# Kernel tuning notes

Measured on AMD Instinct MI355X. Metric: run time of the kernel, lower is better.

Reference implementation:

```python
import jax, jax.numpy as jnp
import numpy as np

EPS = 1e-5

def _layer_norm(x, w):
    mu = jnp.mean(x, axis=-1, keepdims=True)
    var = jnp.mean(jnp.square(x - mu), axis=-1, keepdims=True)
    return (x - mu) * jax.lax.rsqrt(var + EPS) * w

def setup_inputs() -> dict:
    key = jax.random.key(0)
    ks = jax.random.split(key, 5)
    B, T, C, H = 2, 2048, 1024, 16
    std = 0.02
    return {
        "x": jax.random.normal(ks[0], (B, T, C), dtype=jnp.float32),
        "ln1_w": jnp.ones((C,), dtype=jnp.float32),
        "w_attn": jax.random.normal(ks[1], (C, 3 * C), dtype=jnp.float32) * std,
        "w_proj": jax.random.normal(ks[2], (C, C), dtype=jnp.float32) * std,
        "ln2_w": jnp.ones((C,), dtype=jnp.float32),
        "w_fc": jax.random.normal(ks[3], (C, 4 * C), dtype=jnp.float32) * std,
        "w_cproj": jax.random.normal(ks[4], (4 * C, C), dtype=jnp.float32) * std,
    }

def reference(x, ln1_w, w_attn, w_proj, ln2_w, w_fc, w_cproj):
    B, T, C = x.shape
    H = 16
    Dh = C // H
    # --- causal self-attention on ln1(x) ---
    h = _layer_norm(x, ln1_w)
    qkv = h @ w_attn                      # [B,T,3C]
    q, k, v = jnp.split(qkv, 3, axis=-1)
    # [B,T,C] -> [B,H,T,Dh]
    q = q.reshape(B, T, H, Dh).transpose(0, 2, 1, 3)
    k = k.reshape(B, T, H, Dh).transpose(0, 2, 1, 3)
    v = v.reshape(B, T, H, Dh).transpose(0, 2, 1, 3)
    # NOTE: original scales by full embed dim C**-0.5, not head_dim**-0.5
    scores = jnp.einsum('bhqd,bhkd->bhqk', q, k) * (C ** -0.5)
    causal = jnp.tril(jnp.ones((T, T), dtype=bool))
    scores = jnp.where(causal, scores, -jnp.inf)
    probs = jax.nn.softmax(scores, axis=-1)  # dropout=0.0 (eval)
    y = jnp.einsum('bhqk,bhkd->bhqd', probs, v)
    y = y.transpose(0, 2, 1, 3).reshape(B, T, C)
    x = x + y @ w_proj
    # --- MLP on ln2(x) ---
    h = _layer_norm(x, ln2_w)
    x = x + jax.nn.relu(h @ w_fc) @ w_cproj
    return x
```

## Files before the change

### kernel.cpp

```cpp
#include <hip/hip_runtime.h>

typedef __attribute__((ext_vector_type(8))) __bf16 bf16x8;
typedef __attribute__((ext_vector_type(4))) float f32x4;
typedef __attribute__((ext_vector_type(8))) unsigned short u16x8;
typedef __attribute__((ext_vector_type(4))) unsigned short u16x4;
typedef unsigned short u16;

__device__ __forceinline__ u16 f2bf(float f) {
  return __builtin_bit_cast(u16, (__bf16)f);
}
__device__ __forceinline__ float bf2f(u16 u) {
  return __builtin_bit_cast(float, ((unsigned)u) << 16);
}

__device__ __forceinline__ f32x4 mfma16(bf16x8 a, bf16x8 b, f32x4 c) {
  return __builtin_amdgcn_mfma_f32_16x16x32_bf16(a, b, c, 0, 0, 0);
}

__device__ __forceinline__ void gl_lds16(const void* g, void* l) {
  __builtin_amdgcn_global_load_lds(
      (const __attribute__((address_space(1))) unsigned int*)g,
      (__attribute__((address_space(3))) unsigned int*)l, 16, 0, 0);
}

__device__ __forceinline__ f32x4 fmax4(f32x4 a, f32x4 b) {
  f32x4 r;
  r[0] = fmaxf(a[0], b[0]); r[1] = fmaxf(a[1], b[1]);
  r[2] = fmaxf(a[2], b[2]); r[3] = fmaxf(a[3], b[3]);
  return r;
}

__global__ __launch_bounds__(256) void convT_all(const float* __restrict__ w0,
                                                 u16* __restrict__ o0,
                                                 const float* __restrict__ w1,
                                                 u16* __restrict__ o1,
                                                 const float* __restrict__ w2,
                                                 u16* __restrict__ o2,
                                                 const float* __restrict__ w3,
                                                 u16* __restrict__ o3) {
  __shared__ float tile[64][65];
  const int id = blockIdx.x;
  const float* in;
  u16* outT;
  int K, N, bx, by;
  if (id < 768) { in = w0; outT = o0; K = 1024; N = 3072; bx = id & 15; by = id >> 4; }
  else if (id < 1024) { const int j = id - 768; in = w1; outT = o1; K = 1024; N = 1024; bx = j & 15; by = j >> 4; }
  else if (id < 2048) { const int j = id - 1024; in = w2; outT = o2; K = 1024; N = 4096; bx = j & 15; by = j >> 4; }
  else { const int j = id - 2048; in = w3; outT = o3; K = 4096; N = 1024; bx = j & 63; by = j >> 6; }
  const int t = threadIdx.x;
  const int tk = bx * 64, tn = by * 64;
  const int lk = t >> 4, ln = (t & 15) * 4;
#pragma unroll
  for (int r = 0; r < 4; ++r) {
    const int k = lk + r * 16;
    const float4 v = *(const float4*)(in + (size_t)(tk + k) * N + tn + ln);
    tile[k][ln + 0] = v.x; tile[k][ln + 1] = v.y;
    tile[k][ln + 2] = v.z; tile[k][ln + 3] = v.w;
  }
  __syncthreads();
  const int sn = t >> 2, sk = (t & 3) * 4;
#pragma unroll
  for (int j = 0; j < 4; ++j) {
    const int k = sk + j * 16;
    ushort4 o;
    o.x = f2bf(tile[k + 0][sn]); o.y = f2bf(tile[k + 1][sn]);
    o.z = f2bf(tile[k + 2][sn]); o.w = f2bf(tile[k + 3][sn]);
    *(ushort4*)(outT + (size_t)(tn + sn) * K + tk + k) = o;
  }
}

__global__ __launch_bounds__(256) void vtrans(const u16* __restrict__ qkvb,
                                              u16* __restrict__ vT) {
  __shared__ u16 tile[64][72];
  const int t = threadIdx.x;
  const int tt0 = blockIdx.x * 64;
  const int bh = blockIdx.y;
  const int b = bh >> 4, h = bh & 15;
  const u16* src = qkvb + (size_t)(b * 2048 + tt0) * 3072 + 2048 + h * 64;
  {
    const int tl = t >> 2, d0 = (t & 3) * 16;
    const u16x8 a0 = *(const u16x8*)(src + (size_t)tl * 3072 + d0);
    const u16x8 a1 = *(const u16x8*)(src + (size_t)tl * 3072 + d0 + 8);
    *(u16x8*)(&tile[tl][d0]) = a0;
    *(u16x8*)(&tile[tl][d0 + 8]) = a1;
  }
  __syncthreads();
  {
    const int dh = t >> 2, t0 = (t & 3) * 16;
    u16x8 o0, o1;
#pragma unroll
    for (int jj = 0; jj < 8; ++jj) {
      o0[jj] = tile[t0 + jj][dh];
      o1[jj] = tile[t0 + 8 + jj][dh];
    }
    u16* dst = vT + ((size_t)bh * 64 + dh) * 2048 + tt0 + t0;
    *(u16x8*)dst = o0;
    *(u16x8*)(dst + 8) = o1;
  }
}

__global__ __launch_bounds__(256) void ln_bf16(const float* __restrict__ x,
                                               const float* __restrict__ wgt,
                                               u16* __restrict__ out) {
  const int row = blockIdx.x, t = threadIdx.x;
  const float4 v = ((const float4*)(x + (size_t)row * 1024))[t];
  float s = v.x + v.y + v.z + v.w;
  float q = v.x * v.x + v.y * v.y + v.z * v.z + v.w * v.w;
#pragma unroll
  for (int d = 32; d; d >>= 1) { s += __shfl_xor(s, d); q += __shfl_xor(q, d); }
  __shared__ float sb[8];
  const int wv = t >> 6;
  if ((t & 63) == 0) { sb[wv] = s; sb[4 + wv] = q; }
  __syncthreads();
  s = sb[0] + sb[1] + sb[2] + sb[3];
  q = sb[4] + sb[5] + sb[6] + sb[7];
  const float mu = s * (1.f / 1024.f);
  const float rstd = rsqrtf(q * (1.f / 1024.f) - mu * mu + 1e-5f);
  const float4 w4 = ((const float4*)wgt)[t];
  ushort4 o;
  o.x = f2bf((v.x - mu) * rstd * w4.x);
  o.y = f2bf((v.y - mu) * rstd * w4.y);
  o.z = f2bf((v.z - mu) * rstd * w4.z);
  o.w = f2bf((v.w - mu) * rstd * w4.w);
  *(ushort4*)(out + (size_t)row * 1024 + t * 4) = o;
}

__global__ __launch_bounds__(256) void reduce_ln(const float* __restrict__ x,
                                                 const u16* __restrict__ p, int nseg,
                                                 const float* __restrict__ wgt,
                                                 float* __restrict__ x1,
                                                 u16* __restrict__ h2) {
  const int row = blockIdx.x, t = threadIdx.x;
  const size_t ro = (size_t)row * 1024 + t * 4;
  float4 v = *(const float4*)(x + ro);
  for (int sgm = 0; sgm < nseg; ++sgm) {
    const ushort4 u = *(const ushort4*)(p + (size_t)sgm * 4096 * 1024 + ro);
    v.x += bf2f(u.x); v.y += bf2f(u.y); v.z += bf2f(u.z); v.w += bf2f(u.w);
  }
  *(float4*)(x1 + ro) = v;
  float s = v.x + v.y + v.z + v.w;
  float q = v.x * v.x + v.y * v.y + v.z * v.z + v.w * v.w;
#pragma unroll
  for (int d = 32; d; d >>= 1) { s += __shfl_xor(s, d); q += __shfl_xor(q, d); }
  __shared__ float sb[8];
  const int wv = t >> 6;
  if ((t & 63) == 0) { sb[wv] = s; sb[4 + wv] = q; }
  __syncthreads();
  s = sb[0] + sb[1] + sb[2] + sb[3];
  q = sb[4] + sb[5] + sb[6] + sb[7];
  const float mu = s * (1.f / 1024.f);
  const float rstd = rsqrtf(q * (1.f / 1024.f) - mu * mu + 1e-5f);
  const float4 w4 = ((const float4*)wgt)[t];
  ushort4 o;
  o.x = f2bf((v.x - mu) * rstd * w4.x);
  o.y = f2bf((v.y - mu) * rstd * w4.y);
  o.z = f2bf((v.z - mu) * rstd * w4.z);
  o.w = f2bf((v.w - mu) * rstd * w4.w);
  *(ushort4*)(h2 + ro) = o;
}

__global__ __launch_bounds__(256) void reduce_out(const float* __restrict__ x1,
                                                  const u16* __restrict__ p, int nseg,
                                                  float* __restrict__ out) {
  const int i = blockIdx.x * blockDim.x + threadIdx.x;
  const size_t ro = (size_t)i * 4;
  float4 v = *(const float4*)(x1 + ro);
  for (int sgm = 0; sgm < nseg; ++sgm) {
    const ushort4 u = *(const ushort4*)(p + (size_t)sgm * 4096 * 1024 + ro);
    v.x += bf2f(u.x); v.y += bf2f(u.y); v.z += bf2f(u.z); v.w += bf2f(u.w);
  }
  *(float4*)(out + ro) = v;
}

template <int EPI>
__global__ __launch_bounds__(256) void gemm128(const u16* __restrict__ A,
                                               const u16* __restrict__ Bt,
                                               void* __restrict__ outp,
                                               int M, int N, int K) {
  __shared__ u16 As[2][4096];
  __shared__ u16 Bs[2][4096];
  const unsigned gx = gridDim.x, gy = gridDim.y, gxy = gx * gy;
  const unsigned nwg = gxy * gridDim.z;
  unsigned f = (blockIdx.z * gy + blockIdx.y) * gx + blockIdx.x;
  if ((nwg & 7u) == 0u) { const unsigned qq = nwg >> 3; f = (f & 7u) * qq + (f >> 3); }
  const int bx = f % gx, by = (f / gx) % gy, bz = f / gxy;

  const int t = threadIdx.x, w = t >> 6, l = t & 63;
  const int lr = l & 15, g = l >> 4;
  const int row0 = by * 128, col0 = bx * 128;
  const int segK = K / gridDim.z;
  const int k0 = bz * segK, kend = k0 + segK;
  const int wr = w >> 1, wc = w & 1;
  f32x4 acc[4][4] = {};

  const int sr = t >> 2;
  const int sk = (((t & 3) ^ (sr & 3)) << 3);
  const u16* Ag = A + (size_t)(row0 + sr) * K + sk;
  const u16* Bg = Bt + (size_t)(col0 + sr) * K + sk;
  const size_t rstride = (size_t)64 * K;

  auto stage = [&](int kt, int bb) {
    u16* AsW = As[bb] + w * 512;
    u16* BsW = Bs[bb] + w * 512;
    gl_lds16(Ag + kt, AsW);
    gl_lds16(Ag + kt + rstride, AsW + 2048);
    gl_lds16(Bg + kt, BsW);
    gl_lds16(Bg + kt + rstride, BsW + 2048);
  };

  const int gsw = (g ^ (lr & 3)) * 8;

  stage(k0, 0);
  __syncthreads();
  int cur = 0;
  for (int kt = k0; kt < kend; kt += 32) {
    if (kt + 32 < kend) stage(kt + 32, cur ^ 1);
    bf16x8 af[4], bfr[4];
#pragma unroll
    for (int m = 0; m < 4; ++m)
      af[m] = *(const bf16x8*)(As[cur] + (wr * 64 + m * 16 + lr) * 32 + gsw);
#pragma unroll
    for (int n = 0; n < 4; ++n)
      bfr[n] = *(const bf16x8*)(Bs[cur] + (wc * 64 + n * 16 + lr) * 32 + gsw);
#pragma unroll
    for (int m = 0; m < 4; ++m)
#pragma unroll
      for (int n = 0; n < 4; ++n) acc[m][n] = mfma16(af[m], bfr[n], acc[m][n]);
    __syncthreads();
    cur ^= 1;
  }

  const size_t segoff = (size_t)bz * M * N;
#pragma unroll
  for (int m = 0; m < 4; ++m)
#pragma unroll
    for (int n = 0; n < 4; ++n)
#pragma unroll
      for (int r = 0; r < 4; ++r) {
        const int row = row0 + wr * 64 + m * 16 + g * 4 + r;
        const int col = col0 + wc * 64 + n * 16 + lr;
        const size_t idx = (size_t)row * N + col;
        const float v = acc[m][n][r];
        if constexpr (EPI == 0) ((u16*)outp)[idx] = f2bf(v);
        else if constexpr (EPI == 2) ((u16*)outp)[idx] = f2bf(fmaxf(v, 0.f));
        else ((u16*)outp)[segoff + idx] = f2bf(v);
      }
}

template <int EPI>
__global__ __launch_bounds__(512, 2) void gemm256(const u16* __restrict__ A,
                                                  const u16* __restrict__ Bt,
                                                  u16* __restrict__ outp,
                                                  int M, int N, int K) {
  __shared__ u16 S[2][32768];
  const unsigned gx = gridDim.x, gy = gridDim.y, gxy = gx * gy;
  const unsigned nwg = gxy * gridDim.z;
  unsigned f = (blockIdx.z * gy + blockIdx.y) * gx + blockIdx.x;
  if ((nwg & 7u) == 0u) { const unsigned qq = nwg >> 3; f = (f & 7u) * qq + (f >> 3); }
  const int bx = f % gx, by = (f / gx) % gy, bz = f / gxy;
  const int t = threadIdx.x, w = t >> 6, l = t & 63;
  const int lr = l & 15, g = l >> 4;
  const int wr = w >> 2, wc = w & 3;
  const int row0 = by * 256, col0 = bx * 256;
  const int segK = K / gridDim.z;
  const int k0 = bz * segK;
  const int NT = segK >> 6;

  f32x4 acc[8][4] = {};

  const int jr0 = t >> 2;
  const int jr1 = jr0 + 128;
  const int jks = ((t & 3) ^ (jr0 & 3)) << 3;
  auto stage_half = [&](int ht, int idx) {
    const int buf = ht & 1;
    u16* db = &S[buf][(idx & 1) * 16384 + (idx >> 1) * 8192 + w * 512];
    const u16* gb = (idx & 1) ? Bt : A;
    const int rc0 = (idx & 1) ? col0 : row0;
    const int kb = k0 + ht * 64 + (idx >> 1) * 32;
    gl_lds16(gb + (size_t)(rc0 + jr0) * K + kb + jks, db);
    gl_lds16(gb + (size_t)(rc0 + jr1) * K + kb + jks, db + 4096);
  };

  const int gsw = (g ^ (lr & 3)) * 8;

  stage_half(0, 0); stage_half(0, 1); stage_half(0, 2); stage_half(0, 3);
  stage_half(1, 0); stage_half(1, 1);
  asm volatile("s_waitcnt vmcnt(4)" ::: "memory");
  __builtin_amdgcn_s_barrier();

  for (int T = 0; T < NT; ++T) {
    const int cur = T & 1;
    const u16* Ab = &S[cur][0];
    const u16* Bb = &S[cur][16384];
    bf16x8 bfr[4];
#pragma unroll
    for (int sub = 0; sub < 4; ++sub) {
      const int mq = sub & 1, ks = sub >> 1;
      if (mq == 0) {
#pragma unroll
        for (int n = 0; n < 4; ++n)
          bfr[n] = *(const bf16x8*)(Bb + ks * 8192 + (wc * 64 + n * 16 + lr) * 32 + gsw);
      }
      bf16x8 af[4];
#pragma unroll
      for (int m = 0; m < 4; ++m)
        af[m] = *(const bf16x8*)(Ab + ks * 8192 +
                                 (wr * 128 + mq * 64 + m * 16 + lr) * 32 + gsw);
      if (sub < 2) { if (T + 1 < NT) stage_half(T + 1, 2 + sub); }
      else         { if (T + 2 < NT) stage_half(T + 2, sub - 2); }
      __builtin_amdgcn_s_barrier();
      __builtin_amdgcn_s_setprio(1);
#pragma unroll
      for (int m = 0; m < 4; ++m)
#pragma unroll
        for (int n = 0; n < 4; ++n)
          acc[mq * 4 + m][n] = mfma16(af[m], bfr[n], acc[mq * 4 + m][n]);
      __builtin_amdgcn_s_setprio(0);
      if (sub == 3) asm volatile("s_waitcnt vmcnt(4)" ::: "memory");
      __builtin_amdgcn_s_barrier();
    }
  }

  const size_t segoff = (size_t)bz * M * N;
#pragma unroll
  for (int m = 0; m < 8; ++m)
#pragma unroll
    for (int n = 0; n < 4; ++n)
#pragma unroll
      for (int r = 0; r < 4; ++r) {
        const int row = row0 + wr * 128 + m * 16 + g * 4 + r;
        const int col = col0 + wc * 64 + n * 16 + lr;
        const size_t idx = (size_t)row * N + col;
        const float v = acc[m][n][r];
        if constexpr (EPI == 0) outp[idx] = f2bf(v);
        else if constexpr (EPI == 2) outp[idx] = f2bf(fmaxf(v, 0.f));
        else outp[segoff + idx] = f2bf(v);
      }
}

__global__ __launch_bounds__(256) void attn_fwd(const u16* __restrict__ qkvb,
                                                const u16* __restrict__ vT,
                                                u16* __restrict__ y) {
  __shared__ u16 Ks[2][4096];
  __shared__ u16 Vs[2][4096];
  __shared__ u16 Pb[4][16 * 64];
  const int t = threadIdx.x, w = t >> 6, l = t & 63;
  const int lr = l & 15, g = l >> 4;
  const unsigned f = blockIdx.y * gridDim.x + blockIdx.x;
  const int xcd = f & 7, j = f >> 3;
  const int bh = xcd + 8 * (j & 3);
  const int qt = 31 - (j >> 2);
  const int b = bh >> 4, h = bh & 15;
  const size_t base = (size_t)b * 2048 * 3072;
  const u16* Kg = qkvb + base + 1024 + h * 64;
  const u16* Vg = vT + (size_t)bh * 64 * 2048;
  u16* Pw = &Pb[w][0];
  const int pkey = (lr & 7) << 3;
  const float SCL = 0.0450842200277855f;

  auto stageK = [&](int kv0, int bb) {
#pragma unroll
    for (int r = 0; r < 2; ++r) {
      const int dl = (r * 256 + t) * 16;
      const int row = dl >> 7;
      const int srcb = (dl & 127) ^ ((row & 7) << 4);
      gl_lds16(Kg + (size_t)(kv0 + row) * 3072 + (srcb >> 1),
               (char*)Ks[bb] + r * 4096 + w * 1024);
    }
  };
  auto stageV = [&](int kv0, int bb) {
#pragma unroll
    for (int r = 0; r < 2; ++r) {
      const int dl = (r * 256 + t) * 16;
      const int dh = dl >> 7;
      const int srcb = (dl & 127) ^ ((dh & 7) << 4);
      gl_lds16(Vg + (size_t)dh * 2048 + kv0 + (srcb >> 1),
               (char*)Vs[bb] + r * 4096 + w * 1024);
    }
  };

  const int q0w = qt * 64 + w * 16, nt = qt + 1;
  const u16* Qp = qkvb + base + (size_t)(q0w + lr) * 3072 + h * 64;
  const bf16x8 qf0 = *(const bf16x8*)(Qp + g * 8);
  const bf16x8 qf1 = *(const bf16x8*)(Qp + 32 + g * 8);
  f32x4 o[4] = {};
  float m1 = -1e30f, s1 = 0.f;

  stageK(0, 0);
  stageV(0, 0);
  __syncthreads();

  int ct = 0;
  for (int tt = 0; tt < nt; ++tt) {
    const int kv0 = tt * 64;
    if (tt + 1 < nt) {
      stageK(kv0 + 64, ct ^ 1);
      stageV(kv0 + 64, ct ^ 1);
    }

    const u16* Kbuf = Ks[ct];
    const u16* Vbuf = Vs[ct];
    f32x4 s4[4];
#pragma unroll
    for (int i = 0; i < 4; ++i) {
      const int row = i * 16 + lr;
      const int sw = (row & 7) << 4;
      const bf16x8 k0 = *(const bf16x8*)(Kbuf + row * 64 + (((g * 16) ^ sw) >> 1));
      const bf16x8 k1 = *(const bf16x8*)(Kbuf + row * 64 + (((64 + g * 16) ^ sw) >> 1));
      f32x4 z = {0.f, 0.f, 0.f, 0.f};
      z = mfma16(k0, qf0, z);
      s4[i] = mfma16(k1, qf1, z);
    }
    if (kv0 + 64 > q0w) {
#pragma unroll
      for (int i = 0; i < 4; ++i)
#pragma unroll
        for (int r = 0; r < 4; ++r)
          if (kv0 + i * 16 + g * 4 + r > q0w + lr) s4[i][r] = -1e30f;
    }
    const f32x4 mm = fmax4(fmax4(s4[0], s4[1]), fmax4(s4[2], s4[3]));
    float mx = fmaxf(fmaxf(mm[0], mm[1]), fmaxf(mm[2], mm[3]));
    mx = fmaxf(mx, __shfl_xor(mx, 16));
    mx = fmaxf(mx, __shfl_xor(mx, 32));
    const float mxs = mx * SCL;
    if (!__all(mxs <= m1 + 8.f)) {
      const float mn = fmaxf(m1, mxs);
      const float sc = exp2f(m1 - mn);
      m1 = mn;
      s1 *= sc;
      float scr[4];
#pragma unroll
      for (int r = 0; r < 4; ++r) scr[r] = __shfl(sc, g * 4 + r);
#pragma unroll
      for (int n = 0; n < 4; ++n)
#pragma unroll
        for (int r = 0; r < 4; ++r) o[n][r] *= scr[r];
    }
    float ps = 0.f;
#pragma unroll
    for (int i = 0; i < 4; ++i) {
      u16x4 pk;
#pragma unroll
      for (int r = 0; r < 4; ++r) {
        const float p = exp2f(fmaf(s4[i][r], SCL, -m1));
        ps += p;
        pk[r] = f2bf(p);
      }
      *(u16x4*)(Pw + lr * 64 + ((i * 16 + g * 4) ^ pkey)) = pk;
    }
    s1 += ps;
#pragma unroll
    for (int s = 0; s < 2; ++s) {
      const bf16x8 pa = *(const bf16x8*)(Pw + lr * 64 + ((s * 32 + g * 8) ^ pkey));
#pragma unroll
      for (int n = 0; n < 4; ++n) {
        const int dh = n * 16 + lr;
        const bf16x8 vf = *(const bf16x8*)(
            Vbuf + dh * 64 + (((s * 64 + g * 16) ^ ((dh & 7) << 4)) >> 1));
        o[n] = mfma16(pa, vf, o[n]);
      }
    }
    __syncthreads();
    ct ^= 1;
  }

  float den = s1;
  den += __shfl_xor(den, 16);
  den += __shfl_xor(den, 32);
  const float iv = 1.f / den;
  float ivr[4];
#pragma unroll
  for (int r = 0; r < 4; ++r) ivr[r] = __shfl(iv, g * 4 + r);
#pragma unroll
  for (int n = 0; n < 4; ++n)
#pragma unroll
    for (int r = 0; r < 4; ++r) {
      const int row = q0w + g * 4 + r;
      const int col = h * 64 + n * 16 + lr;
      y[(size_t)(b * 2048 + row) * 1024 + col] = f2bf(o[n][r] * ivr[r]);
    }
}

extern "C" void kernel_launch(void* const* d_in, const int* in_sizes, int n_in,
                              void* d_out, int out_size, void* d_ws, size_t ws_size,
                              hipStream_t stream) {
  const float* x      = (const float*)d_in[0];
  const float* ln1w   = (const float*)d_in[1];
  const float* wattn  = (const float*)d_in[2];
  const float* wproj  = (const float*)d_in[3];
  const float* ln2w   = (const float*)d_in[4];
  const float* wfc    = (const float*)d_in[5];
  const float* wcproj = (const float*)d_in[6];
  float* out = (float*)d_out;
  char* ws = (char*)d_ws;
  const size_t MB = 1024 * 1024;
  u16* qkvb    = (u16*)(ws + 0);
  u16* projP   = (u16*)(ws + 0);
  u16* cprojP  = (u16*)(ws + 0);
  u16* h1      = (u16*)(ws + 24 * MB);
  u16* wcprojT = (u16*)(ws + 32 * MB);
  float* x1    = (float*)(ws + 48 * MB);
  u16* yb      = (u16*)(ws + 64 * MB);
  u16* h2      = (u16*)(ws + 64 * MB);
  u16* vT      = (u16*)(ws + 72 * MB);
  u16* hf      = (u16*)(ws + 72 * MB);
  u16* wattnT  = (u16*)(ws + 104 * MB);
  u16* wprojT  = (u16*)(ws + 110 * MB);
  u16* wfcT    = (u16*)(ws + 112 * MB);

  convT_all<<<3072, 256, 0, stream>>>(wattn, wattnT, wproj, wprojT, wfc, wfcT,
                                      wcproj, wcprojT);

  ln_bf16<<<4096, 256, 0, stream>>>(x, ln1w, h1);
  gemm256<0><<<dim3(12, 16, 1), 512, 0, stream>>>(h1, wattnT, qkvb, 4096, 3072, 1024);
  vtrans<<<dim3(32, 32), 256, 0, stream>>>(qkvb, vT);
  attn_fwd<<<dim3(32, 32), 256, 0, stream>>>(qkvb, vT, yb);
  gemm128<4><<<dim3(8, 32, 4), 256, 0, stream>>>(yb, wprojT, projP, 4096, 1024, 1024);
  reduce_ln<<<4096, 256, 0, stream>>>(x, projP, 4, ln2w, x1, h2);
  gemm256<2><<<dim3(16, 16, 1), 512, 0, stream>>>(h2, wfcT, hf, 4096, 4096, 1024);
  gemm256<4><<<dim3(4, 16, 4), 512, 0, stream>>>(hf, wcprojT, cprojP, 4096, 1024, 4096);
  reduce_out<<<4096, 256, 0, stream>>>(x1, cprojP, 4, out);
}
```

Baseline: 227.6 us.

## Fuse LN1 into weight-prep kernel and write transposed V from QKV GEMM epilogue

LayerNorm-1 now runs as extra blocks inside the weight conversion/transpose kernel, which removes one launch. The QKV GEMM gains an epilogue that stages V tiles through LDS with an XOR swizzle and writes them out already transposed, so the separate vtrans kernel and its re-read of V from global memory go away. In exchange, the V-producing GEMM blocks take on extra LDS traffic and barriers in their epilogue.

```diff
diff --git a/kernel.cpp b/kernel.cpp
--- a/kernel.cpp
+++ b/kernel.cpp
@@ -30,24 +30,52 @@
   return r;
 }
 
-__global__ __launch_bounds__(256) void convT_all(const float* __restrict__ w0,
-                                                 u16* __restrict__ o0,
-                                                 const float* __restrict__ w1,
-                                                 u16* __restrict__ o1,
-                                                 const float* __restrict__ w2,
-                                                 u16* __restrict__ o2,
-                                                 const float* __restrict__ w3,
-                                                 u16* __restrict__ o3) {
+__global__ __launch_bounds__(256) void prep(const float* __restrict__ x,
+                                            const float* __restrict__ ln1w,
+                                            u16* __restrict__ h1,
+                                            const float* __restrict__ w0,
+                                            u16* __restrict__ o0,
+                                            const float* __restrict__ w1,
+                                            u16* __restrict__ o1,
+                                            const float* __restrict__ w2,
+                                            u16* __restrict__ o2,
+                                            const float* __restrict__ w3,
+                                            u16* __restrict__ o3) {
   __shared__ float tile[64][65];
+  __shared__ float sb[8];
   const int id = blockIdx.x;
+  const int t = threadIdx.x;
+  if (id < 4096) {
+    const int row = id;
+    const float4 v = ((const float4*)(x + (size_t)row * 1024))[t];
+    float s = v.x + v.y + v.z + v.w;
+    float q = v.x * v.x + v.y * v.y + v.z * v.z + v.w * v.w;
+#pragma unroll
+    for (int d = 32; d; d >>= 1) { s += __shfl_xor(s, d); q += __shfl_xor(q, d); }
+    const int wv = t >> 6;
+    if ((t & 63) == 0) { sb[wv] = s; sb[4 + wv] = q; }
+    __syncthreads();
+    s = sb[0] + sb[1] + sb[2] + sb[3];
+    q = sb[4] + sb[5] + sb[6] + sb[7];
+    const float mu = s * (1.f / 1024.f);
+    const float rstd = rsqrtf(q * (1.f / 1024.f) - mu * mu + 1e-5f);
+    const float4 w4 = ((const float4*)ln1w)[t];
+    ushort4 o;
+    o.x = f2bf((v.x - mu) * rstd * w4.x);
+    o.y = f2bf((v.y - mu) * rstd * w4.y);
+    o.z = f2bf((v.z - mu) * rstd * w4.z);
+    o.w = f2bf((v.w - mu) * rstd * w4.w);
+    *(ushort4*)(h1 + (size_t)row * 1024 + t * 4) = o;
+    return;
+  }
   const float* in;
   u16* outT;
   int K, N, bx, by;
-  if (id < 768) { in = w0; outT = o0; K = 1024; N = 3072; bx = id & 15; by = id >> 4; }
-  else if (id < 1024) { const int j = id - 768; in = w1; outT = o1; K = 1024; N = 1024; bx = j & 15; by = j >> 4; }
-  else if (id < 2048) { const int j = id - 1024; in = w2; outT = o2; K = 1024; N = 4096; bx = j & 15; by = j >> 4; }
-  else { const int j = id - 2048; in = w3; outT = o3; K = 4096; N = 1024; bx = j & 63; by = j >> 6; }
-  const int t = threadIdx.x;
+  const int cid = id - 4096;
+  if (cid < 768) { in = w0; outT = o0; K = 1024; N = 3072; bx = cid & 15; by = cid >> 4; }
+  else if (cid < 1024) { const int j = cid - 768; in = w1; outT = o1; K = 1024; N = 1024; bx = j & 15; by = j >> 4; }
+  else if (cid < 2048) { const int j = cid - 1024; in = w2; outT = o2; K = 1024; N = 4096; bx = j & 15; by = j >> 4; }
+  else { const int j = cid - 2048; in = w3; outT = o3; K = 4096; N = 1024; bx = j & 63; by = j >> 6; }
   const int tk = bx * 64, tn = by * 64;
   const int lk = t >> 4, ln = (t & 15) * 4;
 #pragma unroll
@@ -67,62 +95,6 @@
     o.z = f2bf(tile[k + 2][sn]); o.w = f2bf(tile[k + 3][sn]);
     *(ushort4*)(outT + (size_t)(tn + sn) * K + tk + k) = o;
   }
-}
-
-__global__ __launch_bounds__(256) void vtrans(const u16* __restrict__ qkvb,
-                                              u16* __restrict__ vT) {
-  __shared__ u16 tile[64][72];
-  const int t = threadIdx.x;
-  const int tt0 = blockIdx.x * 64;
-  const int bh = blockIdx.y;
-  const int b = bh >> 4, h = bh & 15;
-  const u16* src = qkvb + (size_t)(b * 2048 + tt0) * 3072 + 2048 + h * 64;
-  {
-    const int tl = t >> 2, d0 = (t & 3) * 16;
-    const u16x8 a0 = *(const u16x8*)(src + (size_t)tl * 3072 + d0);
-    const u16x8 a1 = *(const u16x8*)(src + (size_t)tl * 3072 + d0 + 8);
-    *(u16x8*)(&tile[tl][d0]) = a0;
-    *(u16x8*)(&tile[tl][d0 + 8]) = a1;
-  }
-  __syncthreads();
-  {
-    const int dh = t >> 2, t0 = (t & 3) * 16;
-    u16x8 o0, o1;
-#pragma unroll
-    for (int jj = 0; jj < 8; ++jj) {
-      o0[jj] = tile[t0 + jj][dh];
-      o1[jj] = tile[t0 + 8 + jj][dh];
-    }
-    u16* dst = vT + ((size_t)bh * 64 + dh) * 2048 + tt0 + t0;
-    *(u16x8*)dst = o0;
-    *(u16x8*)(dst + 8) = o1;
-  }
-}
-
-__global__ __launch_bounds__(256) void ln_bf16(const float* __restrict__ x,
-                                               const float* __restrict__ wgt,
-                                               u16* __restrict__ out) {
-  const int row = blockIdx.x, t = threadIdx.x;
-  const float4 v = ((const float4*)(x + (size_t)row * 1024))[t];
-  float s = v.x + v.y + v.z + v.w;
-  float q = v.x * v.x + v.y * v.y + v.z * v.z + v.w * v.w;
-#pragma unroll
-  for (int d = 32; d; d >>= 1) { s += __shfl_xor(s, d); q += __shfl_xor(q, d); }
-  __shared__ float sb[8];
-  const int wv = t >> 6;
-  if ((t & 63) == 0) { sb[wv] = s; sb[4 + wv] = q; }
-  __syncthreads();
-  s = sb[0] + sb[1] + sb[2] + sb[3];
-  q = sb[4] + sb[5] + sb[6] + sb[7];
-  const float mu = s * (1.f / 1024.f);
-  const float rstd = rsqrtf(q * (1.f / 1024.f) - mu * mu + 1e-5f);
-  const float4 w4 = ((const float4*)wgt)[t];
-  ushort4 o;
-  o.x = f2bf((v.x - mu) * rstd * w4.x);
-  o.y = f2bf((v.y - mu) * rstd * w4.y);
-  o.z = f2bf((v.z - mu) * rstd * w4.z);
-  o.w = f2bf((v.w - mu) * rstd * w4.w);
-  *(ushort4*)(out + (size_t)row * 1024 + t * 4) = o;
 }
 
 __global__ __launch_bounds__(256) void reduce_ln(const float* __restrict__ x,
@@ -251,6 +223,7 @@
 __global__ __launch_bounds__(512, 2) void gemm256(const u16* __restrict__ A,
                                                   const u16* __restrict__ Bt,
                                                   u16* __restrict__ outp,
+                                                  u16* __restrict__ outp2,
                                                   int M, int N, int K) {
   __shared__ u16 S[2][32768];
   const unsigned gx = gridDim.x, gy = gridDim.y, gxy = gx * gy;
@@ -319,6 +292,48 @@
       if (sub == 3) asm volatile("s_waitcnt vmcnt(4)" ::: "memory");
       __builtin_amdgcn_s_barrier();
     }
+  }
+
+  if constexpr (EPI == 5) {
+    if (col0 >= 2048) {
+      __syncthreads();
+      u16* Lw = ((u16*)S) + w * 8192;
+#pragma unroll
+      for (int m = 0; m < 8; ++m)
+#pragma unroll
+        for (int n = 0; n < 4; ++n) {
+          const int cl = n * 16 + lr;
+          const int rl = m * 16 + g * 4;
+          u16x4 pk;
+#pragma unroll
+          for (int r = 0; r < 4; ++r) pk[r] = f2bf(acc[m][n][r]);
+          *(u16x4*)(Lw + cl * 128 + (rl ^ ((cl & 7) << 3))) = pk;
+        }
+      __syncthreads();
+      const int b = row0 >> 11;
+      const int tt0w = (row0 & 2047) + wr * 128;
+#pragma unroll
+      for (int iter = 0; iter < 16; ++iter) {
+        const int cl = iter * 4 + (l >> 4);
+        const int r8 = (l & 15) * 8;
+        const u16x8 vv = *(const u16x8*)(Lw + cl * 128 + (r8 ^ ((cl & 7) << 3)));
+        const int col = col0 + wc * 64 + cl;
+        const int hh = (col - 2048) >> 6, dh = col & 63;
+        *(u16x8*)(outp2 + (((size_t)(b * 16 + hh) * 64 + dh) * 2048 + tt0w + r8)) = vv;
+      }
+    } else {
+#pragma unroll
+      for (int m = 0; m < 8; ++m)
+#pragma unroll
+        for (int n = 0; n < 4; ++n)
+#pragma unroll
+          for (int r = 0; r < 4; ++r) {
+            const int row = row0 + wr * 128 + m * 16 + g * 4 + r;
+            const int col = col0 + wc * 64 + n * 16 + lr;
+            outp[(size_t)row * N + col] = f2bf(acc[m][n][r]);
+          }
+    }
+    return;
   }
 
   const size_t segoff = (size_t)bz * M * N;
@@ -508,16 +523,16 @@
   u16* wprojT  = (u16*)(ws + 110 * MB);
   u16* wfcT    = (u16*)(ws + 112 * MB);
 
-  convT_all<<<3072, 256, 0, stream>>>(wattn, wattnT, wproj, wprojT, wfc, wfcT,
-                                      wcproj, wcprojT);
-
-  ln_bf16<<<4096, 256, 0, stream>>>(x, ln1w, h1);
-  gemm256<0><<<dim3(12, 16, 1), 512, 0, stream>>>(h1, wattnT, qkvb, 4096, 3072, 1024);
-  vtrans<<<dim3(32, 32), 256, 0, stream>>>(qkvb, vT);
+  prep<<<7168, 256, 0, stream>>>(x, ln1w, h1, wattn, wattnT, wproj, wprojT,
+                                 wfc, wfcT, wcproj, wcprojT);
+  gemm256<5><<<dim3(12, 16, 1), 512, 0, stream>>>(h1, wattnT, qkvb, vT,
+                                                  4096, 3072, 1024);
   attn_fwd<<<dim3(32, 32), 256, 0, stream>>>(qkvb, vT, yb);
   gemm128<4><<<dim3(8, 32, 4), 256, 0, stream>>>(yb, wprojT, projP, 4096, 1024, 1024);
   reduce_ln<<<4096, 256, 0, stream>>>(x, projP, 4, ln2w, x1, h2);
-  gemm256<2><<<dim3(16, 16, 1), 512, 0, stream>>>(h2, wfcT, hf, 4096, 4096, 1024);
-  gemm256<4><<<dim3(4, 16, 4), 512, 0, stream>>>(hf, wcprojT, cprojP, 4096, 1024, 4096);
+  gemm256<2><<<dim3(16, 16, 1), 512, 0, stream>>>(h2, wfcT, hf, nullptr,
+                                                  4096, 4096, 1024);
+  gemm256<4><<<dim3(4, 16, 4), 512, 0, stream>>>(hf, wcprojT, cprojP, nullptr,
+                                                 4096, 1024, 4096);
   reduce_out<<<4096, 256, 0, stream>>>(x1, cprojP, 4, out);
 }
```

New measurement: 221.3 us. 2.8% less time.
